# Kernel tuning notes

Measured on AMD Instinct MI355X. Metric: run time of the kernel, lower is better.

The kernel has to match this reference:

```python
import jax, jax.numpy as jnp
import numpy as np

T, B, E, H, V, L = 128, 64, 1024, 1024, 10000, 2  # emb_size must equal hidden_size (see decode layer)


def setup_inputs() -> dict:
    key = jax.random.key(0)
    ks = jax.random.split(key, 8)
    s = 0.05
    return {
        "inputs": jax.random.randint(ks[0], (T, B), 0, V),
        "hidden": jnp.zeros((L, B, H), jnp.float32),
        "emb_table": jax.random.normal(ks[1], (V, E), jnp.float32) * s,
        "Ww": jax.random.normal(ks[2], (L, H, E), jnp.float32) * s,
        "Wb": jnp.zeros((L, H), jnp.float32),
        "Uw": jax.random.normal(ks[3], (L, H, H), jnp.float32) * s,
        "Ub": jnp.zeros((L, H), jnp.float32),
        "Fw": jax.random.normal(ks[4], (L, E, H), jnp.float32) * s,
        "Fb": jnp.zeros((L, E), jnp.float32),
        "Dw": jax.random.normal(ks[5], (V, H), jnp.float32) * s,
        "Db": jnp.zeros((V,), jnp.float32),
    }


def reference(inputs, hidden, emb_table, Ww, Wb, Uw, Ub, Fw, Fb, Dw, Db):
    # Dropout is treated as identity (eval mode) for a deterministic reference.
    emb = emb_table[inputs]                     # [T,B,E]

    # --- timestep 0: true recurrence from the provided initial hidden state ---
    x = emb[0]                                  # [B,E]
    h0 = []
    for l in range(L):
        h = jnp.tanh(x @ Ww[l].T + Wb[l] + hidden[l] @ Uw[l].T + Ub[l])  # [B,H]
        x = jnp.tanh(h @ Fw[l].T + Fb[l])                                # [B,E]
        h0.append(h)
    logits0 = x @ Dw.T + Db                     # [B,V]

    # --- timesteps 1..T-1: faithful to the source's indexing bug, the recurrent
    # input h_previous_ts[l] is ALWAYS the timestep-0 state, so all remaining
    # timesteps are independent and can be batched over time. ---
    x = emb[1:]                                 # [T-1,B,E]
    h_rest = []
    for l in range(L):
        aU = h0[l] @ Uw[l].T + Ub[l]            # [B,H], shared across t>=1
        h = jnp.tanh(jnp.einsum('tbe,he->tbh', x, Ww[l]) + Wb[l] + aU)   # [T-1,B,H]
        x = jnp.tanh(jnp.einsum('tbh,eh->tbe', h, Fw[l]) + Fb[l])        # [T-1,B,E]
        h_rest.append(h)
    logits_rest = jnp.einsum('tbe,ve->tbv', x, Dw) + Db  # [T-1,B,V]

    logits = jnp.concatenate([logits0[None], logits_rest], axis=0)        # [T,B,V]

    # Hidden-state list returned by source: [t0_l0, t0_l1, t1_l0, t1_l1, ...]
    h_all = jnp.concatenate(
        [jnp.stack(h0)[None],                               # [1,L,B,H]
         jnp.stack(h_rest).transpose(1, 0, 2, 3)], axis=0   # [T-1,L,B,H]
    ).reshape(T * L, B, H)
    return logits, h_all
```

## Files before the change

### kernel.cpp

```cpp
#include <hip/hip_runtime.h>
#include <hip/hip_bf16.h>
#include <cstdint>
#include <cstddef>

#define T_DIM 128
#define B_DIM 64
#define E_DIM 1024
#define H_DIM 1024
#define V_DIM 10000
#define L_DIM 2
#define VP    10112
#define MR    8128
#define MRP   8192

typedef __bf16 bf16_t;
typedef bf16_t bf16x8 __attribute__((ext_vector_type(8)));
typedef float  f32x4  __attribute__((ext_vector_type(4)));

__device__ __forceinline__ void g2l16(const void* g, void* l) {
  __builtin_amdgcn_global_load_lds((const __attribute__((address_space(1))) void*)g,
                                   (__attribute__((address_space(3))) void*)l,
                                   16, 0, 0);
}

__device__ __forceinline__ float fast_tanh(float v) {
  v = fminf(15.f, fmaxf(-15.f, v));
  float e = __expf(2.f * v);
  return (e - 1.f) / (e + 1.f);
}

__global__ __launch_bounds__(256)
void gemm_bt(const bf16_t* __restrict__ A, const bf16_t* __restrict__ Bm, int K,
             const float* __restrict__ bias, int Nvalid,
             const float* __restrict__ Z, int do_tanh,
             bf16_t* __restrict__ outb, int outb_stride,
             float* __restrict__ outf, long stride_t, int t_off, int stride_b,
             int Mvalid)
{
  __shared__ alignas(16) bf16_t lA[128 * 32];
  __shared__ alignas(16) bf16_t lB[128 * 32];
  const int tid  = threadIdx.x;
  const int wid  = tid >> 6;
  const int lane = tid & 63;
  const int bm = blockIdx.y, bn = blockIdx.x;

  f32x4 zero = {0.f, 0.f, 0.f, 0.f};
  f32x4 acc[4][4];
#pragma unroll
  for (int i = 0; i < 4; ++i)
#pragma unroll
    for (int j = 0; j < 4; ++j) acc[i][j] = zero;

  const int r0 = tid >> 2;
  const int c4 = tid & 3;
  const bf16_t* gA0 = A  + (size_t)(bm * 128 + r0) * K + c4 * 8;
  const bf16_t* gA1 = gA0 + (size_t)64 * K;
  const bf16_t* gB0 = Bm + (size_t)(bn * 128 + r0) * K + c4 * 8;
  const bf16_t* gB1 = gB0 + (size_t)64 * K;
  char* lAb = (char*)lA;
  char* lBb = (char*)lB;
  char* ldsA0 = lAb + wid * 1024;
  char* ldsA1 = lAb + 4096 + wid * 1024;
  char* ldsB0 = lBb + wid * 1024;
  char* ldsB1 = lBb + 4096 + wid * 1024;

  const int mrow = (wid >> 1) * 64;
  const int ncol = (wid & 1) * 64;
  const int fr = lane & 15;
  const int fq = (lane >> 4) * 16;

  for (int k0 = 0; k0 < K; k0 += 32) {
    __syncthreads();
    g2l16(gA0 + k0, ldsA0);
    g2l16(gA1 + k0, ldsA1);
    g2l16(gB0 + k0, ldsB0);
    g2l16(gB1 + k0, ldsB1);
    __syncthreads();

    bf16x8 af[4], bfv[4];
#pragma unroll
    for (int t = 0; t < 4; ++t) {
      af[t]  = *(const bf16x8*)(lAb + (mrow + t * 16 + fr) * 64 + fq);
      bfv[t] = *(const bf16x8*)(lBb + (ncol + t * 16 + fr) * 64 + fq);
    }
#pragma unroll
    for (int tm = 0; tm < 4; ++tm)
#pragma unroll
      for (int tn = 0; tn < 4; ++tn)
        acc[tm][tn] = __builtin_amdgcn_mfma_f32_16x16x32_bf16(af[tm], bfv[tn], acc[tm][tn], 0, 0, 0);
  }

  const int rb = (lane >> 4) * 4;
  const int cb = lane & 15;
#pragma unroll
  for (int tm = 0; tm < 4; ++tm) {
#pragma unroll
    for (int tn = 0; tn < 4; ++tn) {
      const int col = bn * 128 + ncol + tn * 16 + cb;
      const float bv = (col < Nvalid) ? bias[col] : 0.f;
#pragma unroll
      for (int r = 0; r < 4; ++r) {
        const int row = bm * 128 + mrow + tm * 16 + rb + r;
        float v = acc[tm][tn][r] + bv;
        if (Z) v += Z[(row & 63) * 1024 + col];
        if (do_tanh) v = fast_tanh(v);
        if (outb) outb[(size_t)row * outb_stride + col] = (bf16_t)v;
        if (outf && row < Mvalid && col < Nvalid) {
          long o = ((long)((row >> 6) + t_off)) * stride_t
                 + (long)(row & 63) * stride_b + col;
          outf[o] = v;
        }
      }
    }
  }
}

__global__ void k_f32_to_bf16(const float* __restrict__ s, bf16_t* __restrict__ d, int n) {
  int i = blockIdx.x * 256 + threadIdx.x;
  if (i < n) d[i] = (bf16_t)s[i];
}

__global__ void k_cvt_dw(const float* __restrict__ s, bf16_t* __restrict__ d) {
  int i = blockIdx.x * 256 + threadIdx.x;
  int r = i >> 10, c = i & 1023;
  float v = (r < V_DIM) ? s[r * 1024 + c] : 0.f;
  d[i] = (bf16_t)v;
}

__global__ void k_gather_rest(const int* __restrict__ inp, const float* __restrict__ etab,
                              bf16_t* __restrict__ X0) {
  size_t i = (size_t)blockIdx.x * 256 + threadIdx.x;
  int m = (int)(i >> 10), e = (int)(i & 1023);
  float v = 0.f;
  if (m < MR) {
    int t = (m >> 6) + 1, b = m & 63;
    int idx = inp[t * B_DIM + b];
    v = etab[(size_t)idx * E_DIM + e];
  }
  X0[i] = (bf16_t)v;
}

__global__ void k_gather_first(const int* __restrict__ inp, const float* __restrict__ etab,
                               bf16_t* __restrict__ x0) {
  int i = blockIdx.x * 256 + threadIdx.x;
  int m = i >> 10, e = i & 1023;
  float v = 0.f;
  if (m < B_DIM) v = etab[(size_t)inp[m] * E_DIM + e];
  x0[i] = (bf16_t)v;
}

__global__ void k_cvt_hidden(const float* __restrict__ hid, bf16_t* __restrict__ d) {
  int i = blockIdx.x * 256 + threadIdx.x;
  int l = i >> 17, r = (i >> 10) & 127, e = i & 1023;
  float v = (r < B_DIM) ? hid[(l * B_DIM + r) * H_DIM + e] : 0.f;
  d[i] = (bf16_t)v;
}

extern "C" void kernel_launch(void* const* d_in, const int* in_sizes, int n_in,
                              void* d_out, int out_size, void* d_ws, size_t ws_size,
                              hipStream_t stream) {
  const int*   inp    = (const int*)  d_in[0];
  const float* hidden = (const float*)d_in[1];
  const float* etab   = (const float*)d_in[2];
  const float* Ww     = (const float*)d_in[3];
  const float* Wb     = (const float*)d_in[4];
  const float* Uw     = (const float*)d_in[5];
  const float* Ub     = (const float*)d_in[6];
  const float* Fw     = (const float*)d_in[7];
  const float* Fb     = (const float*)d_in[8];
  const float* Dw     = (const float*)d_in[9];
  const float* Db     = (const float*)d_in[10];
  float* out = (float*)d_out;

  char* p = (char*)d_ws;
  auto carve = [&](size_t n) { char* r = p; p += (n + 255) & ~(size_t)255; return r; };
  bf16_t* Wbf  = (bf16_t*)carve((size_t)L_DIM * H_DIM * E_DIM * 2);
  bf16_t* Ubf  = (bf16_t*)carve((size_t)L_DIM * H_DIM * H_DIM * 2);
  bf16_t* Fbf  = (bf16_t*)carve((size_t)L_DIM * E_DIM * H_DIM * 2);
  bf16_t* Dbf  = (bf16_t*)carve((size_t)VP * H_DIM * 2);
  bf16_t* X0   = (bf16_t*)carve((size_t)MRP * E_DIM * 2);
  bf16_t* Hb   = (bf16_t*)carve((size_t)MRP * H_DIM * 2);
  bf16_t* Xb   = (bf16_t*)carve((size_t)MRP * E_DIM * 2);
  bf16_t* s0   = (bf16_t*)carve((size_t)128 * E_DIM * 2);
  bf16_t* s1   = (bf16_t*)carve((size_t)128 * E_DIM * 2);
  bf16_t* h0b0 = (bf16_t*)carve((size_t)128 * H_DIM * 2);
  bf16_t* h0b1 = (bf16_t*)carve((size_t)128 * H_DIM * 2);
  bf16_t* hidb = (bf16_t*)carve((size_t)L_DIM * 128 * H_DIM * 2);
  float*  HU   = (float*) carve((size_t)B_DIM * H_DIM * 4);
  float*  aU0  = (float*) carve((size_t)B_DIM * H_DIM * 4);
  float*  aU1  = (float*) carve((size_t)B_DIM * H_DIM * 4);

  const int WN = L_DIM * H_DIM * E_DIM;
  k_f32_to_bf16<<<(WN + 255) / 256, 256, 0, stream>>>(Ww, Wbf, WN);
  k_f32_to_bf16<<<(WN + 255) / 256, 256, 0, stream>>>(Uw, Ubf, WN);
  k_f32_to_bf16<<<(WN + 255) / 256, 256, 0, stream>>>(Fw, Fbf, WN);
  k_cvt_dw   <<<(VP * H_DIM) / 256, 256, 0, stream>>>(Dw, Dbf);
  k_gather_rest <<<(MRP * E_DIM) / 256, 256, 0, stream>>>(inp, etab, X0);
  k_gather_first<<<(128 * E_DIM) / 256, 256, 0, stream>>>(inp, etab, s0);
  k_cvt_hidden  <<<(L_DIM * 128 * H_DIM) / 256, 256, 0, stream>>>(hidden, hidb);

  float* hall = out + (size_t)T_DIM * B_DIM * V_DIM;
  const long ST_H = (long)L_DIM * B_DIM * H_DIM;
  const long ST_V = (long)B_DIM * V_DIM;

  bf16_t* xc = s0;
  for (int l = 0; l < L_DIM; ++l) {
    bf16_t* h0b = l ? h0b1 : h0b0;
    float*  aU  = l ? aU1 : aU0;
    bf16_t* xn  = l ? s0 : s1;
    gemm_bt<<<dim3(8, 1), 256, 0, stream>>>(hidb + (size_t)l * 128 * H_DIM,
        Ubf + (size_t)l * H_DIM * H_DIM, H_DIM,
        Ub + l * H_DIM, H_DIM, nullptr, 0,
        nullptr, 0, HU, 0L, 0, H_DIM, B_DIM);
    gemm_bt<<<dim3(8, 1), 256, 0, stream>>>(xc,
        Wbf + (size_t)l * H_DIM * E_DIM, E_DIM,
        Wb + l * H_DIM, H_DIM, HU, 1,
        h0b, H_DIM, hall + (size_t)l * B_DIM * H_DIM, ST_H, 0, H_DIM, B_DIM);
    gemm_bt<<<dim3(8, 1), 256, 0, stream>>>(h0b,
        Ubf + (size_t)l * H_DIM * H_DIM, H_DIM,
        Ub + l * H_DIM, H_DIM, nullptr, 0,
        nullptr, 0, aU, 0L, 0, H_DIM, B_DIM);
    gemm_bt<<<dim3(8, 1), 256, 0, stream>>>(h0b,
        Fbf + (size_t)l * E_DIM * H_DIM, H_DIM,
        Fb + l * E_DIM, E_DIM, nullptr, 1,
        xn, E_DIM, nullptr, 0L, 0, 0, 0);
    xc = xn;
  }
  gemm_bt<<<dim3(VP / 128, 1), 256, 0, stream>>>(xc, Dbf, H_DIM,
      Db, V_DIM, nullptr, 0,
      nullptr, 0, out, ST_V, 0, V_DIM, B_DIM);

  bf16_t* Xc = X0;
  for (int l = 0; l < L_DIM; ++l) {
    float* aU = l ? aU1 : aU0;
    gemm_bt<<<dim3(8, MRP / 128), 256, 0, stream>>>(Xc,
        Wbf + (size_t)l * H_DIM * E_DIM, E_DIM,
        Wb + l * H_DIM, H_DIM, aU, 1,
        Hb, H_DIM, hall + (size_t)l * B_DIM * H_DIM, ST_H, 1, H_DIM, MR);
    bf16_t* Xn = l ? X0 : Xb;
    gemm_bt<<<dim3(8, MRP / 128), 256, 0, stream>>>(Hb,
        Fbf + (size_t)l * E_DIM * H_DIM, H_DIM,
        Fb + l * E_DIM, E_DIM, nullptr, 1,
        Xn, E_DIM, nullptr, 0L, 0, 0, 0);
    Xc = Xn;
  }
  gemm_bt<<<dim3(VP / 128, MRP / 128), 256, 0, stream>>>(Xc, Dbf, H_DIM,
      Db, V_DIM, nullptr, 0,
      nullptr, 0, out, ST_V, 1, V_DIM, MR);

  (void)in_sizes; (void)n_in; (void)out_size; (void)ws_size;
}
```

Baseline: 1.200 ms.

## Merge timestep-0 into batched GEMMs, XCD-aware tiling, vectorized conversions

Timestep 0 is folded into the main batched GEMMs: rows 0-63 use a per-row Z buffer holding the real hidden-state term, and rows 64+ use the shared aU term, so the separate small decode and layer launches go away. The two initial U GEMMs are batched into one launch, and the weight-conversion and gather kernels are merged and vectorized to 4 elements per thread. The large GEMMs use a 1D grid remapped so each XCD gets a contiguous band of M tiles for L2 reuse, and the small GEMMs use BK=64. The main cost targeted is launch overhead and redundant small-M GEMM passes, at the price of more complex indexing; Z row selection relies on the in-place Xc update being ordered correctly.

```diff
diff --git a/kernel.cpp b/kernel.cpp
--- a/kernel.cpp
+++ b/kernel.cpp
@@ -9,12 +9,14 @@
 #define H_DIM 1024
 #define V_DIM 10000
 #define L_DIM 2
-#define VP    10112
-#define MR    8128
-#define MRP   8192
+#define VP2   10240
+#define MROWS 8192
+#define WN    2097152
+#define WL    1048576
 
 typedef __bf16 bf16_t;
 typedef bf16_t bf16x8 __attribute__((ext_vector_type(8)));
+typedef bf16_t bf16x4 __attribute__((ext_vector_type(4)));
 typedef float  f32x4  __attribute__((ext_vector_type(4)));
 
 __device__ __forceinline__ void g2l16(const void* g, void* l) {
@@ -29,20 +31,38 @@
   return (e - 1.f) / (e + 1.f);
 }
 
+template<int BK>
 __global__ __launch_bounds__(256)
 void gemm_bt(const bf16_t* __restrict__ A, const bf16_t* __restrict__ Bm, int K,
              const float* __restrict__ bias, int Nvalid,
              const float* __restrict__ Z, int do_tanh,
              bf16_t* __restrict__ outb, int outb_stride,
-             float* __restrict__ outf, long stride_t, int t_off, int stride_b,
-             int Mvalid)
+             float* __restrict__ outf, long stride_t, int stride_b, int Mvalid,
+             int BNT, long abatch, long bbatch, long biasbatch, long obatch)
 {
-  __shared__ alignas(16) bf16_t lA[128 * 32];
-  __shared__ alignas(16) bf16_t lB[128 * 32];
+  __shared__ alignas(16) bf16_t lA[128 * BK];
+  __shared__ alignas(16) bf16_t lB[128 * BK];
   const int tid  = threadIdx.x;
   const int wid  = tid >> 6;
   const int lane = tid & 63;
-  const int bm = blockIdx.y, bn = blockIdx.x;
+
+  int bm, bn;
+  if (BNT > 0) {
+    int g   = blockIdx.x;
+    int SM  = (gridDim.x / BNT) >> 3;
+    int xcd = g & 7;
+    int q   = g >> 3;
+    bm = xcd * SM + (q % SM);
+    bn = q / SM;
+  } else {
+    bn = blockIdx.x;
+    bm = 0;
+    int batch = blockIdx.y;
+    A    += (size_t)batch * abatch;
+    Bm   += (size_t)batch * bbatch;
+    bias += (size_t)batch * biasbatch;
+    if (outf) outf += (size_t)batch * obatch;
+  }
 
   f32x4 zero = {0.f, 0.f, 0.f, 0.f};
   f32x4 acc[4][4];
@@ -51,43 +71,49 @@
 #pragma unroll
     for (int j = 0; j < 4; ++j) acc[i][j] = zero;
 
-  const int r0 = tid >> 2;
-  const int c4 = tid & 3;
-  const bf16_t* gA0 = A  + (size_t)(bm * 128 + r0) * K + c4 * 8;
-  const bf16_t* gA1 = gA0 + (size_t)64 * K;
-  const bf16_t* gB0 = Bm + (size_t)(bn * 128 + r0) * K + c4 * 8;
-  const bf16_t* gB1 = gB0 + (size_t)64 * K;
-  char* lAb = (char*)lA;
-  char* lBb = (char*)lB;
-  char* ldsA0 = lAb + wid * 1024;
-  char* ldsA1 = lAb + 4096 + wid * 1024;
-  char* ldsB0 = lBb + wid * 1024;
-  char* ldsB1 = lBb + 4096 + wid * 1024;
+  constexpr int CW    = BK / 8;
+  constexpr int CALLS = (128 * BK / 8) / 256;
+  const bf16_t* gA[CALLS];
+  const bf16_t* gB[CALLS];
+  int ldsoff[CALLS];
+#pragma unroll
+  for (int u = 0; u < CALLS; ++u) {
+    int chunk = (u * 4 + wid) * 64 + lane;
+    int row = chunk / CW, cc = chunk % CW;
+    gA[u] = A  + (size_t)(bm * 128 + row) * K + cc * 8;
+    gB[u] = Bm + (size_t)(bn * 128 + row) * K + cc * 8;
+    ldsoff[u] = chunk * 16;
+  }
 
   const int mrow = (wid >> 1) * 64;
   const int ncol = (wid & 1) * 64;
   const int fr = lane & 15;
   const int fq = (lane >> 4) * 16;
-
-  for (int k0 = 0; k0 < K; k0 += 32) {
+  char* lAb = (char*)lA;
+  char* lBb = (char*)lB;
+
+  for (int k0 = 0; k0 < K; k0 += BK) {
     __syncthreads();
-    g2l16(gA0 + k0, ldsA0);
-    g2l16(gA1 + k0, ldsA1);
-    g2l16(gB0 + k0, ldsB0);
-    g2l16(gB1 + k0, ldsB1);
+#pragma unroll
+    for (int u = 0; u < CALLS; ++u) g2l16(gA[u] + k0, lAb + ldsoff[u]);
+#pragma unroll
+    for (int u = 0; u < CALLS; ++u) g2l16(gB[u] + k0, lBb + ldsoff[u]);
     __syncthreads();
 
-    bf16x8 af[4], bfv[4];
-#pragma unroll
-    for (int t = 0; t < 4; ++t) {
-      af[t]  = *(const bf16x8*)(lAb + (mrow + t * 16 + fr) * 64 + fq);
-      bfv[t] = *(const bf16x8*)(lBb + (ncol + t * 16 + fr) * 64 + fq);
+#pragma unroll
+    for (int kk = 0; kk < BK / 32; ++kk) {
+      bf16x8 af[4], bfv[4];
+#pragma unroll
+      for (int t = 0; t < 4; ++t) {
+        af[t]  = *(const bf16x8*)(lAb + (mrow + t * 16 + fr) * (2 * BK) + kk * 64 + fq);
+        bfv[t] = *(const bf16x8*)(lBb + (ncol + t * 16 + fr) * (2 * BK) + kk * 64 + fq);
+      }
+#pragma unroll
+      for (int tm = 0; tm < 4; ++tm)
+#pragma unroll
+        for (int tn = 0; tn < 4; ++tn)
+          acc[tm][tn] = __builtin_amdgcn_mfma_f32_16x16x32_bf16(af[tm], bfv[tn], acc[tm][tn], 0, 0, 0);
     }
-#pragma unroll
-    for (int tm = 0; tm < 4; ++tm)
-#pragma unroll
-      for (int tn = 0; tn < 4; ++tn)
-        acc[tm][tn] = __builtin_amdgcn_mfma_f32_16x16x32_bf16(af[tm], bfv[tn], acc[tm][tn], 0, 0, 0);
   }
 
   const int rb = (lane >> 4) * 4;
@@ -102,12 +128,14 @@
       for (int r = 0; r < 4; ++r) {
         const int row = bm * 128 + mrow + tm * 16 + rb + r;
         float v = acc[tm][tn][r] + bv;
-        if (Z) v += Z[(row & 63) * 1024 + col];
+        if (Z) {
+          int zr = (row < 64) ? row : 64 + (row & 63);
+          v += Z[zr * 1024 + col];
+        }
         if (do_tanh) v = fast_tanh(v);
         if (outb) outb[(size_t)row * outb_stride + col] = (bf16_t)v;
         if (outf && row < Mvalid && col < Nvalid) {
-          long o = ((long)((row >> 6) + t_off)) * stride_t
-                 + (long)(row & 63) * stride_b + col;
+          long o = (long)(row >> 6) * stride_t + (long)(row & 63) * stride_b + col;
           outf[o] = v;
         }
       }
@@ -115,45 +143,57 @@
   }
 }
 
-__global__ void k_f32_to_bf16(const float* __restrict__ s, bf16_t* __restrict__ d, int n) {
-  int i = blockIdx.x * 256 + threadIdx.x;
-  if (i < n) d[i] = (bf16_t)s[i];
-}
-
-__global__ void k_cvt_dw(const float* __restrict__ s, bf16_t* __restrict__ d) {
-  int i = blockIdx.x * 256 + threadIdx.x;
-  int r = i >> 10, c = i & 1023;
-  float v = (r < V_DIM) ? s[r * 1024 + c] : 0.f;
-  d[i] = (bf16_t)v;
-}
-
-__global__ void k_gather_rest(const int* __restrict__ inp, const float* __restrict__ etab,
-                              bf16_t* __restrict__ X0) {
-  size_t i = (size_t)blockIdx.x * 256 + threadIdx.x;
-  int m = (int)(i >> 10), e = (int)(i & 1023);
-  float v = 0.f;
-  if (m < MR) {
-    int t = (m >> 6) + 1, b = m & 63;
-    int idx = inp[t * B_DIM + b];
-    v = etab[(size_t)idx * E_DIM + e];
-  }
-  X0[i] = (bf16_t)v;
-}
-
-__global__ void k_gather_first(const int* __restrict__ inp, const float* __restrict__ etab,
-                               bf16_t* __restrict__ x0) {
-  int i = blockIdx.x * 256 + threadIdx.x;
-  int m = i >> 10, e = i & 1023;
-  float v = 0.f;
-  if (m < B_DIM) v = etab[(size_t)inp[m] * E_DIM + e];
-  x0[i] = (bf16_t)v;
-}
-
-__global__ void k_cvt_hidden(const float* __restrict__ hid, bf16_t* __restrict__ d) {
-  int i = blockIdx.x * 256 + threadIdx.x;
-  int l = i >> 17, r = (i >> 10) & 127, e = i & 1023;
-  float v = (r < B_DIM) ? hid[(l * B_DIM + r) * H_DIM + e] : 0.f;
-  d[i] = (bf16_t)v;
+__global__ void k_cvt3(const float* __restrict__ a, const float* __restrict__ b,
+                       const float* __restrict__ c, bf16_t* __restrict__ da,
+                       bf16_t* __restrict__ db, bf16_t* __restrict__ dc) {
+  int i = blockIdx.x * 256 + threadIdx.x;
+  int j = i << 2;
+  int sel = j >> 21;
+  int loc = j & (WN - 1);
+  const float* s = (sel == 0) ? a : (sel == 1) ? b : c;
+  bf16_t*      d = (sel == 0) ? da : (sel == 1) ? db : dc;
+  f32x4 v = *(const f32x4*)(s + loc);
+  bf16x4 o;
+#pragma unroll
+  for (int k = 0; k < 4; ++k) o[k] = (bf16_t)v[k];
+  *(bf16x4*)(d + loc) = o;
+}
+
+__global__ void k_cvt_dw4(const float* __restrict__ s, bf16_t* __restrict__ d) {
+  int i = blockIdx.x * 256 + threadIdx.x;
+  int j = i << 2;
+  int r = j >> 10, c = j & 1023;
+  f32x4 v = {0.f, 0.f, 0.f, 0.f};
+  if (r < V_DIM) v = *(const f32x4*)(s + (size_t)r * 1024 + c);
+  bf16x4 o;
+#pragma unroll
+  for (int k = 0; k < 4; ++k) o[k] = (bf16_t)v[k];
+  *(bf16x4*)(d + j) = o;
+}
+
+__global__ void k_gather4(const int* __restrict__ inp, const float* __restrict__ etab,
+                          bf16_t* __restrict__ X) {
+  int i = blockIdx.x * 256 + threadIdx.x;
+  int j = i << 2;
+  int r = j >> 10, e = j & 1023;
+  int idx = inp[r];
+  f32x4 v = *(const f32x4*)(etab + (size_t)idx * 1024 + e);
+  bf16x4 o;
+#pragma unroll
+  for (int k = 0; k < 4; ++k) o[k] = (bf16_t)v[k];
+  *(bf16x4*)(X + j) = o;
+}
+
+__global__ void k_cvt_hidden4(const float* __restrict__ hid, bf16_t* __restrict__ d) {
+  int i = blockIdx.x * 256 + threadIdx.x;
+  int j = i << 2;
+  int l = j >> 17, r = (j >> 10) & 127, e = j & 1023;
+  f32x4 v = {0.f, 0.f, 0.f, 0.f};
+  if (r < B_DIM) v = *(const f32x4*)(hid + (size_t)(l * B_DIM + r) * 1024 + e);
+  bf16x4 o;
+#pragma unroll
+  for (int k = 0; k < 4; ++k) o[k] = (bf16_t)v[k];
+  *(bf16x4*)(d + j) = o;
 }
 
 extern "C" void kernel_launch(void* const* d_in, const int* in_sizes, int n_in,
@@ -174,79 +214,52 @@
 
   char* p = (char*)d_ws;
   auto carve = [&](size_t n) { char* r = p; p += (n + 255) & ~(size_t)255; return r; };
-  bf16_t* Wbf  = (bf16_t*)carve((size_t)L_DIM * H_DIM * E_DIM * 2);
-  bf16_t* Ubf  = (bf16_t*)carve((size_t)L_DIM * H_DIM * H_DIM * 2);
-  bf16_t* Fbf  = (bf16_t*)carve((size_t)L_DIM * E_DIM * H_DIM * 2);
-  bf16_t* Dbf  = (bf16_t*)carve((size_t)VP * H_DIM * 2);
-  bf16_t* X0   = (bf16_t*)carve((size_t)MRP * E_DIM * 2);
-  bf16_t* Hb   = (bf16_t*)carve((size_t)MRP * H_DIM * 2);
-  bf16_t* Xb   = (bf16_t*)carve((size_t)MRP * E_DIM * 2);
-  bf16_t* s0   = (bf16_t*)carve((size_t)128 * E_DIM * 2);
-  bf16_t* s1   = (bf16_t*)carve((size_t)128 * E_DIM * 2);
-  bf16_t* h0b0 = (bf16_t*)carve((size_t)128 * H_DIM * 2);
-  bf16_t* h0b1 = (bf16_t*)carve((size_t)128 * H_DIM * 2);
-  bf16_t* hidb = (bf16_t*)carve((size_t)L_DIM * 128 * H_DIM * 2);
-  float*  HU   = (float*) carve((size_t)B_DIM * H_DIM * 4);
-  float*  aU0  = (float*) carve((size_t)B_DIM * H_DIM * 4);
-  float*  aU1  = (float*) carve((size_t)B_DIM * H_DIM * 4);
-
-  const int WN = L_DIM * H_DIM * E_DIM;
-  k_f32_to_bf16<<<(WN + 255) / 256, 256, 0, stream>>>(Ww, Wbf, WN);
-  k_f32_to_bf16<<<(WN + 255) / 256, 256, 0, stream>>>(Uw, Ubf, WN);
-  k_f32_to_bf16<<<(WN + 255) / 256, 256, 0, stream>>>(Fw, Fbf, WN);
-  k_cvt_dw   <<<(VP * H_DIM) / 256, 256, 0, stream>>>(Dw, Dbf);
-  k_gather_rest <<<(MRP * E_DIM) / 256, 256, 0, stream>>>(inp, etab, X0);
-  k_gather_first<<<(128 * E_DIM) / 256, 256, 0, stream>>>(inp, etab, s0);
-  k_cvt_hidden  <<<(L_DIM * 128 * H_DIM) / 256, 256, 0, stream>>>(hidden, hidb);
+  bf16_t* Wbf  = (bf16_t*)carve((size_t)WN * 2);
+  bf16_t* Ubf  = (bf16_t*)carve((size_t)WN * 2);
+  bf16_t* Fbf  = (bf16_t*)carve((size_t)WN * 2);
+  bf16_t* Dbf  = (bf16_t*)carve((size_t)VP2 * 1024 * 2);
+  bf16_t* Xc   = (bf16_t*)carve((size_t)MROWS * 1024 * 2);
+  bf16_t* Hc   = (bf16_t*)carve((size_t)MROWS * 1024 * 2);
+  bf16_t* hidb = (bf16_t*)carve((size_t)L_DIM * 128 * 1024 * 2);
+  bf16_t* h0b  = (bf16_t*)carve((size_t)128 * 1024 * 2);
+  float*  Zbuf = (float*) carve((size_t)2 * 128 * 1024 * 4);
+  float*  Z0 = Zbuf, * Z1 = Zbuf + 131072;
 
   float* hall = out + (size_t)T_DIM * B_DIM * V_DIM;
   const long ST_H = (long)L_DIM * B_DIM * H_DIM;
   const long ST_V = (long)B_DIM * V_DIM;
 
-  bf16_t* xc = s0;
+  k_cvt3       <<<3 * WN / 4 / 256, 256, 0, stream>>>(Ww, Uw, Fw, Wbf, Ubf, Fbf);
+  k_cvt_dw4    <<<VP2 * 1024 / 4 / 256, 256, 0, stream>>>(Dw, Dbf);
+  k_gather4    <<<MROWS * 1024 / 4 / 256, 256, 0, stream>>>(inp, etab, Xc);
+  k_cvt_hidden4<<<L_DIM * 128 * 1024 / 4 / 256, 256, 0, stream>>>(hidden, hidb);
+
+  gemm_bt<64><<<dim3(8, 2), 256, 0, stream>>>(hidb, Ubf, 1024,
+      Ub, 1024, nullptr, 0, nullptr, 0,
+      Zbuf, 0L, 1024, 64,
+      0, (long)128 * 1024, (long)WL, 1024L, 131072L);
+
   for (int l = 0; l < L_DIM; ++l) {
-    bf16_t* h0b = l ? h0b1 : h0b0;
-    float*  aU  = l ? aU1 : aU0;
-    bf16_t* xn  = l ? s0 : s1;
-    gemm_bt<<<dim3(8, 1), 256, 0, stream>>>(hidb + (size_t)l * 128 * H_DIM,
-        Ubf + (size_t)l * H_DIM * H_DIM, H_DIM,
-        Ub + l * H_DIM, H_DIM, nullptr, 0,
-        nullptr, 0, HU, 0L, 0, H_DIM, B_DIM);
-    gemm_bt<<<dim3(8, 1), 256, 0, stream>>>(xc,
-        Wbf + (size_t)l * H_DIM * E_DIM, E_DIM,
-        Wb + l * H_DIM, H_DIM, HU, 1,
-        h0b, H_DIM, hall + (size_t)l * B_DIM * H_DIM, ST_H, 0, H_DIM, B_DIM);
-    gemm_bt<<<dim3(8, 1), 256, 0, stream>>>(h0b,
-        Ubf + (size_t)l * H_DIM * H_DIM, H_DIM,
-        Ub + l * H_DIM, H_DIM, nullptr, 0,
-        nullptr, 0, aU, 0L, 0, H_DIM, B_DIM);
-    gemm_bt<<<dim3(8, 1), 256, 0, stream>>>(h0b,
-        Fbf + (size_t)l * E_DIM * H_DIM, H_DIM,
-        Fb + l * E_DIM, E_DIM, nullptr, 1,
-        xn, E_DIM, nullptr, 0L, 0, 0, 0);
-    xc = xn;
-  }
-  gemm_bt<<<dim3(VP / 128, 1), 256, 0, stream>>>(xc, Dbf, H_DIM,
-      Db, V_DIM, nullptr, 0,
-      nullptr, 0, out, ST_V, 0, V_DIM, B_DIM);
-
-  bf16_t* Xc = X0;
-  for (int l = 0; l < L_DIM; ++l) {
-    float* aU = l ? aU1 : aU0;
-    gemm_bt<<<dim3(8, MRP / 128), 256, 0, stream>>>(Xc,
-        Wbf + (size_t)l * H_DIM * E_DIM, E_DIM,
-        Wb + l * H_DIM, H_DIM, aU, 1,
-        Hb, H_DIM, hall + (size_t)l * B_DIM * H_DIM, ST_H, 1, H_DIM, MR);
-    bf16_t* Xn = l ? X0 : Xb;
-    gemm_bt<<<dim3(8, MRP / 128), 256, 0, stream>>>(Hb,
-        Fbf + (size_t)l * E_DIM * H_DIM, H_DIM,
-        Fb + l * E_DIM, E_DIM, nullptr, 1,
-        Xn, E_DIM, nullptr, 0L, 0, 0, 0);
-    Xc = Xn;
-  }
-  gemm_bt<<<dim3(VP / 128, MRP / 128), 256, 0, stream>>>(Xc, Dbf, H_DIM,
-      Db, V_DIM, nullptr, 0,
-      nullptr, 0, out, ST_V, 1, V_DIM, MR);
+    float* Zl = l ? Z1 : Z0;
+    gemm_bt<64><<<dim3(8, 1), 256, 0, stream>>>(Xc, Wbf + (size_t)l * WL, 1024,
+        Wb + l * 1024, 1024, Zl, 1, h0b, 1024,
+        nullptr, 0L, 0, 0, 0, 0, 0, 0, 0);
+    gemm_bt<64><<<dim3(8, 1), 256, 0, stream>>>(h0b, Ubf + (size_t)l * WL, 1024,
+        Ub + l * 1024, 1024, nullptr, 0, nullptr, 0,
+        Zl + 64 * 1024, 0L, 1024, 64, 0, 0, 0, 0, 0);
+    gemm_bt<32><<<dim3(64 * 8), 256, 0, stream>>>(Xc, Wbf + (size_t)l * WL, 1024,
+        Wb + l * 1024, 1024, Zl, 1, Hc, 1024,
+        hall + (size_t)l * B_DIM * H_DIM, ST_H, 1024, MROWS,
+        8, 0, 0, 0, 0);
+    gemm_bt<32><<<dim3(64 * 8), 256, 0, stream>>>(Hc, Fbf + (size_t)l * WL, 1024,
+        Fb + l * 1024, 1024, nullptr, 1, Xc, 1024,
+        nullptr, 0L, 0, 0, 8, 0, 0, 0, 0);
+  }
+
+  gemm_bt<32><<<dim3(64 * 80), 256, 0, stream>>>(Xc, Dbf, 1024,
+      Db, V_DIM, nullptr, 0, nullptr, 0,
+      out, ST_V, V_DIM, MROWS,
+      80, 0, 0, 0, 0);
 
   (void)in_sizes; (void)n_in; (void)out_size; (void)ws_size;
 }
```

After: 1.083 ms. 1.11x faster.
